# Kernel optimization log

Hardware: AMD Instinct MI355X
Metric: run time of the kernel (lower is better)

## Reference

```python
import jax, jax.numpy as jnp
import numpy as np

# Static problem sizes
B, C, T, H, W = 2, 256, 16, 64, 64
N = 128                      # number of ROIs
OT, OH, OW = 2, 7, 7         # output_size (t, h, w)
SS, TS = 1.0, 1.0            # spatial_scale, temporal_scale
T_EXT_MAX, S_EXT_MAX = 16, 32  # max ROI extents (by construction of rois)
# adaptive_max_pool bin length is bounded by ceil(L/O)+1
KT = (T_EXT_MAX + OT - 1) // OT + 1   # 9
KS = (S_EXT_MAX + OH - 1) // OH + 1   # 6


def setup_inputs() -> dict:
    key = jax.random.key(0)
    features = jax.random.normal(key, (B, C, T, H, W), dtype=jnp.float32)
    rng = np.random.default_rng(0)
    bidx = rng.integers(0, B, N)
    te = rng.integers(4, T_EXT_MAX + 1, N)
    t1 = rng.integers(0, T - te + 1)
    t2 = t1 + te - 1
    he = rng.integers(8, S_EXT_MAX + 1, N)
    y1 = rng.integers(0, H - he + 1)
    y2 = y1 + he - 1
    we = rng.integers(8, S_EXT_MAX + 1, N)
    x1 = rng.integers(0, W - we + 1)
    x2 = x1 + we - 1
    # layout: (batch_idx, t1, x1, y1, t2, x2, y2)
    rois = np.stack([bidx, t1, x1, y1, t2, x2, y2], axis=1).astype(np.float32)
    return {"features": features, "rois": jnp.asarray(rois)}


def _bin_idx(start, length, O, K):
    """Adaptive-pool bin indices for one dim. Returns abs indices [O,K] and validity mask."""
    o = jnp.arange(O)
    s = (o * length) // O                      # floor(o*L/O)
    e = ((o + 1) * length + O - 1) // O        # ceil((o+1)*L/O)
    idx = s[:, None] + jnp.arange(K)[None, :]  # [O, K]
    valid = idx < e[:, None]
    return start + jnp.minimum(idx, length - 1), valid


def _pool_one(roi, features):
    b = roi[0].astype(jnp.int32)
    # source scales coords cols [1,2,3,4] by spatial_scale and [0,5] by temporal_scale
    scale = jnp.array([TS, SS, SS, SS, SS, TS], dtype=roi.dtype)
    c = jnp.floor(roi[1:7] * scale).astype(jnp.int32)
    t1, x1, y1, t2, x2, y2 = c[0], c[1], c[2], c[3], c[4], c[5]
    feat = features[b]  # [C, T, H, W]
    neg = -jnp.inf
    # W dimension
    wi, wv = _bin_idx(x1, x2 - x1 + 1, OW, KS)
    x = feat[:, :, :, wi]                                    # [C,T,H,OW,KS]
    x = jnp.where(wv, x, neg).max(axis=-1)                   # [C,T,H,OW]
    # H dimension
    hi, hv = _bin_idx(y1, y2 - y1 + 1, OH, KS)
    x = jnp.take(x, hi.reshape(-1), axis=2).reshape(C, T, OH, KS, OW)
    x = jnp.where(hv[None, None, :, :, None], x, neg).max(axis=3)  # [C,T,OH,OW]
    # T dimension
    ti, tv = _bin_idx(t1, t2 - t1 + 1, OT, KT)
    x = jnp.take(x, ti.reshape(-1), axis=1).reshape(C, OT, KT, OH, OW)
    return jnp.where(tv[None, :, :, None, None], x, neg).max(axis=2)  # [C,OT,OH,OW]


def reference(features, rois):
    # sequential map over ROIs keeps peak memory bounded (each ROI pool is fully vectorized)
    return jax.lax.map(lambda r: _pool_one(r, features), rois)  # [N,C,OT,OH,OW]
```

## Files before the change

kernel.cpp:

```cpp
#include <hip/hip_runtime.h>
#include <hip/hip_fp16.h>
#include <math.h>

#define BB 2
#define CC 256
#define TT 16
#define HH 64
#define WW 64
#define NN 128
#define OT 2
#define OH 7
#define OW 7
#define PP (TT * HH * WW)
#define BIN (OT * OH * OW)
#define CU2 (CC / 2)
#define NQ (NN * OH * OW)
#define GRIDP (NQ / 2)

#define FEATT_BYTES ((size_t)BB * CC * PP * 2)
#define STAGE_OFF   FEATT_BYTES
#define STAGE_BYTES ((size_t)NN * BIN * CC * 4)
#define PERM_OFF    (STAGE_OFF + ((STAGE_BYTES + 255) & ~(size_t)255))
#define WS_NEED     (PERM_OFF + NN * 4)

typedef _Float16 hf2 __attribute__((ext_vector_type(2)));

__global__ __launch_bounds__(256) void transpose_f16_kernel(
    const float* __restrict__ in, unsigned int* __restrict__ outt )
{
    __shared__ float tile[64][65];
    int pb = blockIdx.x & 1023;
    int cb = (blockIdx.x >> 10) & 3;
    int b  = blockIdx.x >> 12;

    int tx = threadIdx.x & 63;
    int wv = threadIdx.x >> 6;
    const float* src = in + ((size_t)b * CC + cb * 64) * PP + pb * 64;
    #pragma unroll
    for (int r = 0; r < 16; ++r) {
        int c = wv + r * 4;
        tile[tx][c] = src[(size_t)c * PP + tx];
    }
    __syncthreads();

    int cp   = threadIdx.x & 31;
    int prow = threadIdx.x >> 5;
    size_t base = ((size_t)b * PP + (size_t)pb * 64) * CC + cb * 64;
    #pragma unroll
    for (int r = 0; r < 8; ++r) {
        int p = prow + r * 8;
        __half h0 = __float2half(tile[p][2 * cp]);
        __half h1 = __float2half(tile[p][2 * cp + 1]);
        unsigned int u = (unsigned int)__half_as_ushort(h0)
                       | ((unsigned int)__half_as_ushort(h1) << 16);
        outt[(base + (size_t)p * CC) / 2 + cp] = u;
    }
}

__global__ __launch_bounds__(128) void sort_rois_kernel(
    const float* __restrict__ rois, int* __restrict__ perm)
{
    __shared__ unsigned int k[NN];
    int t = threadIdx.x;
    const float* r = rois + t * 7;
    int b  = (int)r[0];
    int t1 = (int)r[1], x1 = (int)r[2], y1 = (int)r[3];
    int t2 = (int)r[4], x2 = (int)r[5], y2 = (int)r[6];
    int tc = (t1 + t2) >> 1;
    int yc = ((y1 + y2) >> 1) >> 2;
    int xc = ((x1 + x2) >> 1) >> 2;
    unsigned int m = 0;
    #pragma unroll
    for (int i = 0; i < 4; ++i) {
        m |= (((unsigned)(tc >> i) & 1u) << (3 * i + 2));
        m |= (((unsigned)(yc >> i) & 1u) << (3 * i + 1));
        m |= (((unsigned)(xc >> i) & 1u) << (3 * i));
    }
    unsigned int key = ((unsigned)b << 12) | m;
    k[t] = (key << 8) | (unsigned)t;
    __syncthreads();
    for (int kk = 2; kk <= NN; kk <<= 1) {
        for (int j = kk >> 1; j > 0; j >>= 1) {
            int ixj = t ^ j;
            if (ixj > t) {
                bool up = ((t & kk) == 0);
                unsigned int a = k[t], c = k[ixj];
                if ((a > c) == up) { k[t] = c; k[ixj] = a; }
            }
            __syncthreads();
        }
    }
    perm[t] = (int)(k[t] & 0xFFu);
}

template<int NX, int D>
__device__ __forceinline__ void pool_loop(
    const unsigned int* __restrict__ p, int niter, int ny,
    int ystep, int tstep, hf2& m0, hf2& m1, hf2& m2, hf2& m3)
{
    uint4 v[D][NX];
    int iy = 0;

#define PLOAD(d)                                            \
    _Pragma("unroll")                                       \
    for (int j = 0; j < NX; ++j)                            \
        v[d][j] = *(const uint4*)(p + j * CU2);

#define PADV()                                              \
    do { if (++iy == ny) { iy = 0; p += tstep; } else p += ystep; } while (0)

#define PCONS(d)                                            \
    _Pragma("unroll")                                       \
    for (int j = 0; j < NX; ++j) {                          \
        m0 = __builtin_elementwise_max(m0, __builtin_bit_cast(hf2, v[d][j].x)); \
        m1 = __builtin_elementwise_max(m1, __builtin_bit_cast(hf2, v[d][j].y)); \
        m2 = __builtin_elementwise_max(m2, __builtin_bit_cast(hf2, v[d][j].z)); \
        m3 = __builtin_elementwise_max(m3, __builtin_bit_cast(hf2, v[d][j].w)); \
    }

    if (niter > D) {
        #pragma unroll
        for (int d = 0; d < D; ++d) { PLOAD(d); PADV(); }
        int M = (niter - D) / D;
        int r = (niter - D) % D;
        for (int s = 0; s < M; ++s) {
            #pragma unroll
            for (int d = 0; d < D; ++d) { PCONS(d); PLOAD(d); PADV(); }
        }
        #pragma unroll
        for (int d = 0; d < D - 1; ++d)
            if (d < r) { PCONS(d); PLOAD(d); PADV(); }
        #pragma unroll
        for (int d = 0; d < D; ++d) PCONS(d);
    } else {
        for (int i = 0; i < niter; ++i) { PLOAD(0); PADV(); PCONS(0); }
    }
#undef PLOAD
#undef PADV
#undef PCONS
}

__global__ __launch_bounds__(256) void roipool3d_f16_kernel(
    const unsigned int* __restrict__ featt,
    const float* __restrict__ rois,
    const int* __restrict__ perm,
    float* __restrict__ stage)
{
    __shared__ unsigned int comb[2][64][4];

    int wg  = blockIdx.x;
    int swz = (wg & 7) * (GRIDP / 8) + (wg >> 3);
    int wave  = threadIdx.x >> 6;
    int qslot = wave >> 1;
    int tc    = wave & 1;
    int lane = threadIdx.x & 63;
    int half = lane >> 5;
    int cl   = lane & 31;
    int q    = swz * 2 + qslot;
    int rem  = q % (OH * OW);
    int n    = perm[q / (OH * OW)];
    int oh   = rem / OW;
    int ow   = rem % OW;

    const float* r = rois + n * 7;
    int b  = (int)r[0];
    int t1 = (int)r[1];
    int x1 = (int)r[2];
    int y1 = (int)r[3];
    int t2 = (int)r[4];
    int x2 = (int)r[5];
    int y2 = (int)r[6];
    int lt = t2 - t1 + 1, lh = y2 - y1 + 1, lw = x2 - x1 + 1;

    int nt_full = (lt + 1) >> 1;
    int ntc0 = (nt_full + 1) >> 1;
    int nt_c = tc ? (nt_full - ntc0) : ntc0;
    int t0 = t1 + (half ? (lt >> 1) : 0) + (tc ? ntc0 : 0);

    int hs = (oh * lh) / OH, he = ((oh + 1) * lh + OH - 1) / OH;
    int ws = (ow * lw) / OW, we = ((ow + 1) * lw + OW - 1) / OW;
    int ny = he - hs;
    int nx = we - ws;
    int niter = nt_c * ny;

    const unsigned int* p = featt
        + (size_t)((size_t)b * PP + (size_t)((t0 * HH + (y1 + hs)) * WW + (x1 + ws))) * CU2
        + cl * 4;

    const int ystep = WW * CU2;
    const int tstep = (HH - (ny - 1)) * WW * CU2;

    hf2 m0; m0[0] = (_Float16)(-65504.0f); m0[1] = m0[0];
    hf2 m1 = m0, m2 = m0, m3 = m0;

    switch (nx) {
        case 2:  pool_loop<2, 6>(p, niter, ny, ystep, tstep, m0, m1, m2, m3); break;
        case 3:  pool_loop<3, 4>(p, niter, ny, ystep, tstep, m0, m1, m2, m3); break;
        case 4:  pool_loop<4, 3>(p, niter, ny, ystep, tstep, m0, m1, m2, m3); break;
        case 5:  pool_loop<5, 2>(p, niter, ny, ystep, tstep, m0, m1, m2, m3); break;
        default: pool_loop<6, 2>(p, niter, ny, ystep, tstep, m0, m1, m2, m3); break;
    }

    if (tc) {
        comb[qslot][lane][0] = __builtin_bit_cast(unsigned int, m0);
        comb[qslot][lane][1] = __builtin_bit_cast(unsigned int, m1);
        comb[qslot][lane][2] = __builtin_bit_cast(unsigned int, m2);
        comb[qslot][lane][3] = __builtin_bit_cast(unsigned int, m3);
    }
    __syncthreads();
    if (!tc) {
        m0 = __builtin_elementwise_max(m0, __builtin_bit_cast(hf2, comb[qslot][lane][0]));
        m1 = __builtin_elementwise_max(m1, __builtin_bit_cast(hf2, comb[qslot][lane][1]));
        m2 = __builtin_elementwise_max(m2, __builtin_bit_cast(hf2, comb[qslot][lane][2]));
        m3 = __builtin_elementwise_max(m3, __builtin_bit_cast(hf2, comb[qslot][lane][3]));

        int c0 = cl * 8;
        int bin = half * (OH * OW) + rem;
        float4 s0 = { (float)m0[0], (float)m0[1], (float)m1[0], (float)m1[1] };
        float4 s1 = { (float)m2[0], (float)m2[1], (float)m3[0], (float)m3[1] };
        float* sp = stage + ((size_t)n * BIN + bin) * CC + c0;
        *(float4*)sp       = s0;
        *(float4*)(sp + 4) = s1;
    }
}

__global__ __launch_bounds__(128) void untranspose_kernel(
    const float* __restrict__ stage, float* __restrict__ out)
{
    __shared__ float t[32][99];
    int n  = blockIdx.x >> 3;
    int c0 = (blockIdx.x & 7) * 32;
    const float* sp = stage + (size_t)n * BIN * CC + c0;
    for (int k = threadIdx.x; k < BIN * 32; k += 128) {
        int bin = k >> 5, c = k & 31;
        t[c][bin] = sp[(size_t)bin * CC + c];
    }
    __syncthreads();
    float* op = out + ((size_t)n * CC + c0) * BIN;
    for (int c = 0; c < 32; ++c) {
        if (threadIdx.x < BIN)
            op[(size_t)c * BIN + threadIdx.x] = t[c][threadIdx.x];
    }
}

#define NXCD 8
#define C_PER_XCD (CC / NXCD)
#define PLANE (NN * BIN)
#define BLOCKS_PER_C (PLANE / 256)
__global__ __launch_bounds__(256) void roipool3d_fb_kernel(
    const float* __restrict__ feat, const float* __restrict__ rois,
    float* __restrict__ out)
{
    int wg = blockIdx.x, xcd = wg % NXCD, i = wg / NXCD;
    int c = xcd * C_PER_XCD + i / BLOCKS_PER_C;
    int p = (i % BLOCKS_PER_C) * 256 + threadIdx.x;
    int n = p / BIN, rem = p % BIN;
    int ot = rem / (OH * OW), oh = (rem / OW) % OH, ow = rem % OW;
    const float* r = rois + n * 7;
    int b = (int)r[0], t1 = (int)r[1], x1 = (int)r[2], y1 = (int)r[3];
    int t2 = (int)r[4], x2 = (int)r[5], y2 = (int)r[6];
    int lt = t2 - t1 + 1, lh = y2 - y1 + 1, lw = x2 - x1 + 1;
    int ts = (ot * lt) / OT, te = ((ot + 1) * lt + OT - 1) / OT;
    int hs = (oh * lh) / OH, he = ((oh + 1) * lh + OH - 1) / OH;
    int ws = (ow * lw) / OW, we = ((ow + 1) * lw + OW - 1) / OW;
    const float* fbase = feat + ((size_t)b * CC + c) * PP;
    float m = -INFINITY;
    for (int t = t1 + ts; t < t1 + te; ++t)
        for (int y = y1 + hs; y < y1 + he; ++y)
            for (int x = x1 + ws; x < x1 + we; ++x)
                m = fmaxf(m, fbase[t * (HH * WW) + y * WW + x]);
    out[((size_t)n * CC + c) * BIN + rem] = m;
}

extern "C" void kernel_launch(void* const* d_in, const int* in_sizes, int n_in,
                              void* d_out, int out_size, void* d_ws, size_t ws_size,
                              hipStream_t stream) {
    const float* feat = (const float*)d_in[0];
    const float* rois = (const float*)d_in[1];
    float* out = (float*)d_out;

    if (ws_size >= WS_NEED && d_ws) {
        unsigned int* featt = (unsigned int*)d_ws;
        float* stage = (float*)((char*)d_ws + STAGE_OFF);
        int*   perm  = (int*)((char*)d_ws + PERM_OFF);
        sort_rois_kernel<<<1, 128, 0, stream>>>(rois, perm);
        transpose_f16_kernel<<<BB * 4 * 1024, 256, 0, stream>>>(feat, featt);
        roipool3d_f16_kernel<<<GRIDP, 256, 0, stream>>>(featt, rois, perm, stage);
        untranspose_kernel<<<NN * 8, 128, 0, stream>>>(stage, out);
    } else {
        roipool3d_fb_kernel<<<NXCD * C_PER_XCD * BLOCKS_PER_C, 256, 0, stream>>>(
            feat, rois, out);
    }
}
```

Before: 83.54 us.

## Drop ROI sort kernel and deepen load pipelining in pool loop

Removes the single-block bitonic sort kernel that reordered ROIs by a Morton key, so the pool kernel indexes ROIs directly and one launch plus a serial dependency go away. Raises the number of in-flight load stages per nx case, and replaces the serial short-path loop with a fully unrolled batch of loads followed by the max reductions. The risks are higher register pressure from the deeper buffers and the loss of the cache locality the spatial sort provided.

```diff
diff --git a/kernel.cpp b/kernel.cpp
--- a/kernel.cpp
+++ b/kernel.cpp
@@ -20,8 +20,7 @@
 #define FEATT_BYTES ((size_t)BB * CC * PP * 2)
 #define STAGE_OFF   FEATT_BYTES
 #define STAGE_BYTES ((size_t)NN * BIN * CC * 4)
-#define PERM_OFF    (STAGE_OFF + ((STAGE_BYTES + 255) & ~(size_t)255))
-#define WS_NEED     (PERM_OFF + NN * 4)
+#define WS_NEED     (STAGE_OFF + STAGE_BYTES)
 
 typedef _Float16 hf2 __attribute__((ext_vector_type(2)));
 
@@ -57,42 +56,6 @@
     }
 }
 
-__global__ __launch_bounds__(128) void sort_rois_kernel(
-    const float* __restrict__ rois, int* __restrict__ perm)
-{
-    __shared__ unsigned int k[NN];
-    int t = threadIdx.x;
-    const float* r = rois + t * 7;
-    int b  = (int)r[0];
-    int t1 = (int)r[1], x1 = (int)r[2], y1 = (int)r[3];
-    int t2 = (int)r[4], x2 = (int)r[5], y2 = (int)r[6];
-    int tc = (t1 + t2) >> 1;
-    int yc = ((y1 + y2) >> 1) >> 2;
-    int xc = ((x1 + x2) >> 1) >> 2;
-    unsigned int m = 0;
-    #pragma unroll
-    for (int i = 0; i < 4; ++i) {
-        m |= (((unsigned)(tc >> i) & 1u) << (3 * i + 2));
-        m |= (((unsigned)(yc >> i) & 1u) << (3 * i + 1));
-        m |= (((unsigned)(xc >> i) & 1u) << (3 * i));
-    }
-    unsigned int key = ((unsigned)b << 12) | m;
-    k[t] = (key << 8) | (unsigned)t;
-    __syncthreads();
-    for (int kk = 2; kk <= NN; kk <<= 1) {
-        for (int j = kk >> 1; j > 0; j >>= 1) {
-            int ixj = t ^ j;
-            if (ixj > t) {
-                bool up = ((t & kk) == 0);
-                unsigned int a = k[t], c = k[ixj];
-                if ((a > c) == up) { k[t] = c; k[ixj] = a; }
-            }
-            __syncthreads();
-        }
-    }
-    perm[t] = (int)(k[t] & 0xFFu);
-}
-
 template<int NX, int D>
 __device__ __forceinline__ void pool_loop(
     const unsigned int* __restrict__ p, int niter, int ny,
@@ -118,7 +81,14 @@
         m3 = __builtin_elementwise_max(m3, __builtin_bit_cast(hf2, v[d][j].w)); \
     }
 
-    if (niter > D) {
+    if (niter <= D) {
+        #pragma unroll
+        for (int d = 0; d < D; ++d)
+            if (d < niter) { PLOAD(d); PADV(); }
+        #pragma unroll
+        for (int d = 0; d < D; ++d)
+            if (d < niter) { PCONS(d); }
+    } else {
         #pragma unroll
         for (int d = 0; d < D; ++d) { PLOAD(d); PADV(); }
         int M = (niter - D) / D;
@@ -128,12 +98,10 @@
             for (int d = 0; d < D; ++d) { PCONS(d); PLOAD(d); PADV(); }
         }
         #pragma unroll
-        for (int d = 0; d < D - 1; ++d)
+        for (int d = 0; d < D; ++d)
             if (d < r) { PCONS(d); PLOAD(d); PADV(); }
         #pragma unroll
         for (int d = 0; d < D; ++d) PCONS(d);
-    } else {
-        for (int i = 0; i < niter; ++i) { PLOAD(0); PADV(); PCONS(0); }
     }
 #undef PLOAD
 #undef PADV
@@ -143,7 +111,6 @@
 __global__ __launch_bounds__(256) void roipool3d_f16_kernel(
     const unsigned int* __restrict__ featt,
     const float* __restrict__ rois,
-    const int* __restrict__ perm,
     float* __restrict__ stage)
 {
     __shared__ unsigned int comb[2][64][4];
@@ -158,7 +125,7 @@
     int cl   = lane & 31;
     int q    = swz * 2 + qslot;
     int rem  = q % (OH * OW);
-    int n    = perm[q / (OH * OW)];
+    int n    = q / (OH * OW);
     int oh   = rem / OW;
     int ow   = rem % OW;
 
@@ -194,11 +161,11 @@
     hf2 m1 = m0, m2 = m0, m3 = m0;
 
     switch (nx) {
-        case 2:  pool_loop<2, 6>(p, niter, ny, ystep, tstep, m0, m1, m2, m3); break;
-        case 3:  pool_loop<3, 4>(p, niter, ny, ystep, tstep, m0, m1, m2, m3); break;
-        case 4:  pool_loop<4, 3>(p, niter, ny, ystep, tstep, m0, m1, m2, m3); break;
-        case 5:  pool_loop<5, 2>(p, niter, ny, ystep, tstep, m0, m1, m2, m3); break;
-        default: pool_loop<6, 2>(p, niter, ny, ystep, tstep, m0, m1, m2, m3); break;
+        case 2:  pool_loop<2, 8>(p, niter, ny, ystep, tstep, m0, m1, m2, m3); break;
+        case 3:  pool_loop<3, 6>(p, niter, ny, ystep, tstep, m0, m1, m2, m3); break;
+        case 4:  pool_loop<4, 5>(p, niter, ny, ystep, tstep, m0, m1, m2, m3); break;
+        case 5:  pool_loop<5, 4>(p, niter, ny, ystep, tstep, m0, m1, m2, m3); break;
+        default: pool_loop<6, 3>(p, niter, ny, ystep, tstep, m0, m1, m2, m3); break;
     }
 
     if (tc) {
@@ -282,10 +249,8 @@
     if (ws_size >= WS_NEED && d_ws) {
         unsigned int* featt = (unsigned int*)d_ws;
         float* stage = (float*)((char*)d_ws + STAGE_OFF);
-        int*   perm  = (int*)((char*)d_ws + PERM_OFF);
-        sort_rois_kernel<<<1, 128, 0, stream>>>(rois, perm);
         transpose_f16_kernel<<<BB * 4 * 1024, 256, 0, stream>>>(feat, featt);
-        roipool3d_f16_kernel<<<GRIDP, 256, 0, stream>>>(featt, rois, perm, stage);
+        roipool3d_f16_kernel<<<GRIDP, 256, 0, stream>>>(featt, rois, stage);
         untranspose_kernel<<<NN * 8, 128, 0, stream>>>(stage, out);
     } else {
         roipool3d_fb_kernel<<<NXCD * C_PER_XCD * BLOCKS_PER_C, 256, 0, stream>>>(
```

New measurement: 89.70 us. +7.4%, slower.
